# Performance work log

Measured on AMD Instinct MI355X. Metric: run time of the kernel, lower is better.

The kernel has to match this reference:

```python
import jax, jax.numpy as jnp
from jax import lax
import numpy as np

N_FEATURE = 128
EDGE = 12          # int(sqrt(128) + 1)
BATCH = 131072


def maxpool2(x):
    # 2x2 max pool, stride 2, NCHW
    return lax.reduce_window(x, -jnp.inf, lax.max,
                             (1, 1, 2, 2), (1, 1, 2, 2), 'VALID')


def conv3x3(x, w, b):
    # 3x3 conv, padding=1, NCHW / OIHW
    y = lax.conv_general_dilated(x, w, window_strides=(1, 1),
                                 padding=((1, 1), (1, 1)),
                                 dimension_numbers=('NCHW', 'OIHW', 'NCHW'))
    return y + b[None, :, None, None]


def setup_inputs() -> dict:
    key = jax.random.key(0)
    ks = jax.random.split(key, 9)
    x = jax.random.normal(ks[0], (BATCH, N_FEATURE), dtype=jnp.float32)
    conv1_w = jax.random.normal(ks[1], (3, 1, 3, 3), dtype=jnp.float32) * 0.1
    conv1_b = jnp.zeros((3,), dtype=jnp.float32)
    conv2_w = jax.random.normal(ks[2], (6, 3, 3, 3), dtype=jnp.float32) * 0.1
    conv2_b = jnp.zeros((6,), dtype=jnp.float32)
    fc1_w = jax.random.normal(ks[3], (128, 54), dtype=jnp.float32) * 0.1
    fc1_b = jnp.zeros((128,), dtype=jnp.float32)
    out_w = jax.random.normal(ks[4], (N_FEATURE, 128), dtype=jnp.float32) * 0.1
    out_b = jnp.zeros((N_FEATURE,), dtype=jnp.float32)
    return {"x": x, "conv1_w": conv1_w, "conv1_b": conv1_b,
            "conv2_w": conv2_w, "conv2_b": conv2_b,
            "fc1_w": fc1_w, "fc1_b": fc1_b,
            "out_w": out_w, "out_b": out_b}


def reference(x, conv1_w, conv1_b, conv2_w, conv2_b, fc1_w, fc1_b, out_w, out_b):
    num = x.shape[0]
    n = x.shape[1]                       # 128
    pad = EDGE * EDGE - n                # 16 trailing zeros
    # vectorized transto3D: row-major fill of edge x edge grid, zero-padded tail
    g = jnp.pad(x, ((0, 0), (0, pad))).reshape(num, 1, EDGE, EDGE)
    h = jax.nn.relu(maxpool2(conv3x3(g, conv1_w, conv1_b)))      # [num,3,6,6]
    h = jax.nn.relu(maxpool2(conv3x3(h, conv2_w, conv2_b)))      # [num,6,3,3]
    h = h.reshape(num, 54)
    h = jax.nn.relu(h @ fc1_w.T + fc1_b)                         # [num,128]
    return h @ out_w.T + out_b                                   # [num,128]
```

## Files before the change

kernel.cpp:

```cpp
#include <hip/hip_runtime.h>

typedef unsigned int uint;
typedef unsigned short ushort;

using bf16x8 = __attribute__((ext_vector_type(8))) short;
using f32x4  = __attribute__((ext_vector_type(4))) float;

__device__ __forceinline__ float b2f(ushort u) {
  union { uint i; float f; } v; v.i = ((uint)u) << 16; return v.f;
}
__device__ __forceinline__ ushort f2b(float f) {
  union { float f; uint i; } v; v.f = f;
  uint r = (v.i + 0x7fffu + ((v.i >> 16) & 1u)) >> 16;
  return (ushort)r;
}
__device__ __forceinline__ bf16x8 ldfrag(const ushort* p) {
  union { uint4 u; bf16x8 v; } x; x.u = *(const uint4*)p; return x.v;
}

__global__ __launch_bounds__(256, 1) void conv_kernel(
    const float* __restrict__ x,
    const float* __restrict__ w1g, const float* __restrict__ b1g,
    const float* __restrict__ w2g, const float* __restrict__ b2g,
    ushort* __restrict__ h2ws) {
  const int s = blockIdx.x * 256 + threadIdx.x;
  const float* xs = x + (size_t)s * 128;

  float xv[128];
#pragma unroll
  for (int i = 0; i < 32; ++i) {
    const float4 v = ((const float4*)xs)[i];
    xv[4 * i + 0] = v.x; xv[4 * i + 1] = v.y;
    xv[4 * i + 2] = v.z; xv[4 * i + 3] = v.w;
  }

  float w1[3][9], b1[3];
#pragma unroll
  for (int c = 0; c < 3; ++c) {
    b1[c] = b1g[c];
#pragma unroll
    for (int q = 0; q < 9; ++q) w1[c][q] = w1g[c * 9 + q];
  }

  float h1[3][6][6];
#pragma unroll
  for (int pr = 0; pr < 6; ++pr)
#pragma unroll
    for (int pc = 0; pc < 6; ++pc)
#pragma unroll
      for (int ch = 0; ch < 3; ++ch) {
        float m = -3.0e38f;
#pragma unroll
        for (int dr = 0; dr < 2; ++dr)
#pragma unroll
          for (int dc = 0; dc < 2; ++dc) {
            float a = 0.f;
#pragma unroll
            for (int ky = 0; ky < 3; ++ky)
#pragma unroll
              for (int kx = 0; kx < 3; ++kx) {
                const int r = 2 * pr + dr + ky - 1;
                const int c = 2 * pc + dc + kx - 1;
                if (r >= 0 && r < 12 && c >= 0 && c < 12 && (12 * r + c) < 128)
                  a = fmaf(w1[ch][ky * 3 + kx], xv[12 * r + c], a);
              }
            m = fmaxf(m, a);
          }
        h1[ch][pr][pc] = fmaxf(m + b1[ch], 0.f);
      }

  float h2[54];
#pragma unroll
  for (int o = 0; o < 6; ++o) {
    float w2[27];
#pragma unroll
    for (int q = 0; q < 27; ++q) w2[q] = w2g[o * 27 + q];
    const float bo = b2g[o];
#pragma unroll
    for (int qr = 0; qr < 3; ++qr)
#pragma unroll
      for (int qc = 0; qc < 3; ++qc) {
        float m = -3.0e38f;
#pragma unroll
        for (int dr = 0; dr < 2; ++dr)
#pragma unroll
          for (int dc = 0; dc < 2; ++dc) {
            float a = 0.f;
#pragma unroll
            for (int i = 0; i < 3; ++i)
#pragma unroll
              for (int ky = 0; ky < 3; ++ky)
#pragma unroll
                for (int kx = 0; kx < 3; ++kx) {
                  const int yy = 2 * qr + dr + ky - 1;
                  const int xx = 2 * qc + dc + kx - 1;
                  if (yy >= 0 && yy < 6 && xx >= 0 && xx < 6)
                    a = fmaf(w2[i * 9 + ky * 3 + kx], h1[i][yy][xx], a);
                }
            m = fmaxf(m, a);
          }
        h2[o * 9 + qr * 3 + qc] = fmaxf(m + bo, 0.f);
      }
  }

  uint pk[32];
#pragma unroll
  for (int q = 0; q < 27; ++q)
    pk[q] = (uint)f2b(h2[2 * q]) | ((uint)f2b(h2[2 * q + 1]) << 16);
#pragma unroll
  for (int q = 27; q < 32; ++q) pk[q] = 0u;
  uint4* dst = (uint4*)(h2ws + (size_t)s * 64);
#pragma unroll
  for (int i = 0; i < 8; ++i) {
    uint4 v; v.x = pk[4 * i]; v.y = pk[4 * i + 1];
    v.z = pk[4 * i + 2]; v.w = pk[4 * i + 3];
    dst[i] = v;
  }
}

__global__ __launch_bounds__(256, 2) void fc_kernel(
    const ushort* __restrict__ h2ws,
    const float* __restrict__ fc1w, const float* __restrict__ fc1b,
    const float* __restrict__ outw, const float* __restrict__ outb,
    float* __restrict__ out) {
  __shared__ __align__(16) union {
    struct { ushort h2s[128][72]; ushort w1s[128][72]; } p1;
    struct { ushort tA[128][136]; ushort owB[128][136]; } p2;
  } U;
  __shared__ float fb1[128], ob[128];

  const int t = threadIdx.x;
  const int s0 = blockIdx.x * 128;
  const int lane = t & 63, wv = t >> 6;
  const int quad = lane >> 4, lm = lane & 15;

  if (t < 128) { fb1[t] = fc1b[t]; ob[t] = outb[t]; }

#pragma unroll
  for (int i = 0; i < 4; ++i) {
    const int f = t + 256 * i;
    const int si = f >> 3, kb = f & 7;
    *(uint4*)&U.p1.h2s[si][kb * 8] =
        *(const uint4*)(h2ws + (size_t)(s0 + si) * 64 + kb * 8);
  }
#pragma unroll
  for (int i = 0; i < 27; ++i) {
    const int f = t + 256 * i;
    const int n = f / 54, k = f - 54 * n;
    U.p1.w1s[n][k] = f2b(fc1w[f]);
  }
  if (t < 128) {
    uint* p = (uint*)&U.p1.w1s[t][54];
#pragma unroll
    for (int q = 0; q < 5; ++q) p[q] = 0u;
  }
  __syncthreads();

  f32x4 acc[2][8];
#pragma unroll
  for (int mt = 0; mt < 2; ++mt)
#pragma unroll
    for (int nt = 0; nt < 8; ++nt) acc[mt][nt] = (f32x4){0.f, 0.f, 0.f, 0.f};

#pragma unroll
  for (int kk = 0; kk < 2; ++kk) {
    const int ko = kk * 32 + quad * 8;
    bf16x8 a[2], b[8];
#pragma unroll
    for (int mt = 0; mt < 2; ++mt)
      a[mt] = ldfrag(&U.p1.h2s[32 * wv + 16 * mt + lm][ko]);
#pragma unroll
    for (int nt = 0; nt < 8; ++nt)
      b[nt] = ldfrag(&U.p1.w1s[16 * nt + lm][ko]);
#pragma unroll
    for (int mt = 0; mt < 2; ++mt)
#pragma unroll
      for (int nt = 0; nt < 8; ++nt)
        acc[mt][nt] = __builtin_amdgcn_mfma_f32_16x16x32_bf16(
            a[mt], b[nt], acc[mt][nt], 0, 0, 0);
  }
  __syncthreads();

#pragma unroll
  for (int mt = 0; mt < 2; ++mt)
#pragma unroll
    for (int nt = 0; nt < 8; ++nt) {
      const int col = 16 * nt + lm;
      const float bj = fb1[col];
#pragma unroll
      for (int r = 0; r < 4; ++r) {
        const int row = 32 * wv + 16 * mt + quad * 4 + r;
        U.p2.tA[row][col] = f2b(fmaxf(acc[mt][nt][r] + bj, 0.f));
      }
    }
#pragma unroll
  for (int i = 0; i < 16; ++i) {
    const int f = t + 256 * i;
    const int o = f >> 5, j4 = (f & 31) * 4;
    const float4 v = *(const float4*)(outw + o * 128 + j4);
    uint2 pv;
    pv.x = (uint)f2b(v.x) | ((uint)f2b(v.y) << 16);
    pv.y = (uint)f2b(v.z) | ((uint)f2b(v.w) << 16);
    *(uint2*)&U.p2.owB[o][j4] = pv;
  }
  __syncthreads();

  f32x4 acc2[2][8];
#pragma unroll
  for (int mt = 0; mt < 2; ++mt)
#pragma unroll
    for (int nt = 0; nt < 8; ++nt) acc2[mt][nt] = (f32x4){0.f, 0.f, 0.f, 0.f};

#pragma unroll
  for (int kk = 0; kk < 4; ++kk) {
    const int ko = kk * 32 + quad * 8;
    bf16x8 a[2], b[8];
#pragma unroll
    for (int mt = 0; mt < 2; ++mt)
      a[mt] = ldfrag(&U.p2.tA[32 * wv + 16 * mt + lm][ko]);
#pragma unroll
    for (int nt = 0; nt < 8; ++nt)
      b[nt] = ldfrag(&U.p2.owB[16 * nt + lm][ko]);
#pragma unroll
    for (int mt = 0; mt < 2; ++mt)
#pragma unroll
      for (int nt = 0; nt < 8; ++nt)
        acc2[mt][nt] = __builtin_amdgcn_mfma_f32_16x16x32_bf16(
            a[mt], b[nt], acc2[mt][nt], 0, 0, 0);
  }

#pragma unroll
  for (int mt = 0; mt < 2; ++mt)
#pragma unroll
    for (int nt = 0; nt < 8; ++nt) {
      const int col = 16 * nt + lm;
      const float bo = ob[col];
#pragma unroll
      for (int r = 0; r < 4; ++r) {
        const int srow = s0 + 32 * wv + 16 * mt + quad * 4 + r;
        out[(size_t)srow * 128 + col] = acc2[mt][nt][r] + bo;
      }
    }
}

extern "C" void kernel_launch(void* const* d_in, const int* in_sizes, int n_in,
                              void* d_out, int out_size, void* d_ws, size_t ws_size,
                              hipStream_t stream) {
  const float* x    = (const float*)d_in[0];
  const float* w1   = (const float*)d_in[1];
  const float* b1   = (const float*)d_in[2];
  const float* w2   = (const float*)d_in[3];
  const float* b2   = (const float*)d_in[4];
  const float* fc1w = (const float*)d_in[5];
  const float* fc1b = (const float*)d_in[6];
  const float* outw = (const float*)d_in[7];
  const float* outb = (const float*)d_in[8];
  float* outp = (float*)d_out;
  ushort* ws  = (ushort*)d_ws;

  const int N = in_sizes[0] / 128;

  conv_kernel<<<N / 256, 256, 0, stream>>>(x, w1, b1, w2, b2, ws);
  fc_kernel<<<N / 128, 256, 0, stream>>>(ws, fc1w, fc1b, outw, outb, outp);
}
```

Baseline: 169.0 us.

## Fuse conv and FC stages into one kernel with pre-converted bf16 weights

Merges the conv kernel and the FC kernel into a single kernel that stages the pooled conv features in shared memory instead of a global workspace, then runs both MFMA GEMMs over two 128-row halves. A one-block prep kernel converts the fc1 and out weights to bf16 once per call, and the GEMM B fragments are read straight from global/L2 rather than staged in LDS. This removes the h2 global round trip and the per-block weight conversion. In exchange, the fused kernel needs more registers and LDS, which may lower occupancy, and the B-fragment loads now hit global memory.

After: 171.4 us. No clear change (+1.4%).

```diff
diff --git a/kernel.cpp b/kernel.cpp
--- a/kernel.cpp
+++ b/kernel.cpp
@@ -6,9 +6,6 @@
 using bf16x8 = __attribute__((ext_vector_type(8))) short;
 using f32x4  = __attribute__((ext_vector_type(4))) float;
 
-__device__ __forceinline__ float b2f(ushort u) {
-  union { uint i; float f; } v; v.i = ((uint)u) << 16; return v.f;
-}
 __device__ __forceinline__ ushort f2b(float f) {
   union { float f; uint i; } v; v.f = f;
   uint r = (v.i + 0x7fffu + ((v.i >> 16) & 1u)) >> 16;
@@ -18,229 +15,215 @@
   union { uint4 u; bf16x8 v; } x; x.u = *(const uint4*)p; return x.v;
 }
 
-__global__ __launch_bounds__(256, 1) void conv_kernel(
+__global__ __launch_bounds__(256) void prep_kernel(
+    const float* __restrict__ fc1w, const float* __restrict__ outw,
+    ushort* __restrict__ ws) {
+  const int t = threadIdx.x;
+#pragma unroll
+  for (int i = 0; i < 32; ++i) {
+    const int idx = t * 32 + i;
+    const int row = idx >> 6, k = idx & 63;
+    ws[idx] = (k < 54) ? f2b(fc1w[row * 54 + k]) : (ushort)0;
+  }
+#pragma unroll
+  for (int i = 0; i < 64; ++i) {
+    const int idx = t * 64 + i;
+    ws[8192 + idx] = f2b(outw[idx]);
+  }
+}
+
+__global__ __launch_bounds__(256, 2) void fused_kernel(
     const float* __restrict__ x,
     const float* __restrict__ w1g, const float* __restrict__ b1g,
     const float* __restrict__ w2g, const float* __restrict__ b2g,
-    ushort* __restrict__ h2ws) {
-  const int s = blockIdx.x * 256 + threadIdx.x;
-  const float* xs = x + (size_t)s * 128;
-
-  float xv[128];
-#pragma unroll
-  for (int i = 0; i < 32; ++i) {
-    const float4 v = ((const float4*)xs)[i];
-    xv[4 * i + 0] = v.x; xv[4 * i + 1] = v.y;
-    xv[4 * i + 2] = v.z; xv[4 * i + 3] = v.w;
-  }
-
-  float w1[3][9], b1[3];
-#pragma unroll
-  for (int c = 0; c < 3; ++c) {
-    b1[c] = b1g[c];
-#pragma unroll
-    for (int q = 0; q < 9; ++q) w1[c][q] = w1g[c * 9 + q];
-  }
-
-  float h1[3][6][6];
-#pragma unroll
-  for (int pr = 0; pr < 6; ++pr)
-#pragma unroll
-    for (int pc = 0; pc < 6; ++pc)
-#pragma unroll
-      for (int ch = 0; ch < 3; ++ch) {
-        float m = -3.0e38f;
-#pragma unroll
-        for (int dr = 0; dr < 2; ++dr)
-#pragma unroll
-          for (int dc = 0; dc < 2; ++dc) {
-            float a = 0.f;
-#pragma unroll
-            for (int ky = 0; ky < 3; ++ky)
-#pragma unroll
-              for (int kx = 0; kx < 3; ++kx) {
-                const int r = 2 * pr + dr + ky - 1;
-                const int c = 2 * pc + dc + kx - 1;
-                if (r >= 0 && r < 12 && c >= 0 && c < 12 && (12 * r + c) < 128)
-                  a = fmaf(w1[ch][ky * 3 + kx], xv[12 * r + c], a);
-              }
-            m = fmaxf(m, a);
-          }
-        h1[ch][pr][pc] = fmaxf(m + b1[ch], 0.f);
-      }
-
-  float h2[54];
-#pragma unroll
-  for (int o = 0; o < 6; ++o) {
-    float w2[27];
-#pragma unroll
-    for (int q = 0; q < 27; ++q) w2[q] = w2g[o * 27 + q];
-    const float bo = b2g[o];
-#pragma unroll
-    for (int qr = 0; qr < 3; ++qr)
-#pragma unroll
-      for (int qc = 0; qc < 3; ++qc) {
-        float m = -3.0e38f;
-#pragma unroll
-        for (int dr = 0; dr < 2; ++dr)
-#pragma unroll
-          for (int dc = 0; dc < 2; ++dc) {
-            float a = 0.f;
-#pragma unroll
-            for (int i = 0; i < 3; ++i)
+    const ushort* __restrict__ wsw,
+    const float* __restrict__ fc1b, const float* __restrict__ outb,
+    float* __restrict__ out) {
+  __shared__ __align__(16) ushort h2A[256][72];
+  __shared__ __align__(16) ushort tA[128][136];
+  __shared__ float fb1[128], ob[128];
+
+  const int t = threadIdx.x;
+  const int s0 = blockIdx.x * 256;
+
+  if (t < 128) { fb1[t] = fc1b[t]; ob[t] = outb[t]; }
+
+  {
+    const float* xs = x + (size_t)(s0 + t) * 128;
+    float xv[128];
+#pragma unroll
+    for (int i = 0; i < 32; ++i) {
+      const float4 v = ((const float4*)xs)[i];
+      xv[4 * i + 0] = v.x; xv[4 * i + 1] = v.y;
+      xv[4 * i + 2] = v.z; xv[4 * i + 3] = v.w;
+    }
+
+    float w1[3][9], b1[3];
+#pragma unroll
+    for (int c = 0; c < 3; ++c) {
+      b1[c] = b1g[c];
+#pragma unroll
+      for (int q = 0; q < 9; ++q) w1[c][q] = w1g[c * 9 + q];
+    }
+
+    float h1[3][6][6];
+#pragma unroll
+    for (int pr = 0; pr < 6; ++pr)
+#pragma unroll
+      for (int pc = 0; pc < 6; ++pc)
+#pragma unroll
+        for (int ch = 0; ch < 3; ++ch) {
+          float m = -3.0e38f;
+#pragma unroll
+          for (int dr = 0; dr < 2; ++dr)
+#pragma unroll
+            for (int dc = 0; dc < 2; ++dc) {
+              float a = 0.f;
 #pragma unroll
               for (int ky = 0; ky < 3; ++ky)
 #pragma unroll
                 for (int kx = 0; kx < 3; ++kx) {
-                  const int yy = 2 * qr + dr + ky - 1;
-                  const int xx = 2 * qc + dc + kx - 1;
-                  if (yy >= 0 && yy < 6 && xx >= 0 && xx < 6)
-                    a = fmaf(w2[i * 9 + ky * 3 + kx], h1[i][yy][xx], a);
+                  const int r = 2 * pr + dr + ky - 1;
+                  const int c = 2 * pc + dc + kx - 1;
+                  if (r >= 0 && r < 12 && c >= 0 && c < 12 && (12 * r + c) < 128)
+                    a = fmaf(w1[ch][ky * 3 + kx], xv[12 * r + c], a);
                 }
-            m = fmaxf(m, a);
-          }
-        h2[o * 9 + qr * 3 + qc] = fmaxf(m + bo, 0.f);
-      }
-  }
-
-  uint pk[32];
-#pragma unroll
-  for (int q = 0; q < 27; ++q)
-    pk[q] = (uint)f2b(h2[2 * q]) | ((uint)f2b(h2[2 * q + 1]) << 16);
-#pragma unroll
-  for (int q = 27; q < 32; ++q) pk[q] = 0u;
-  uint4* dst = (uint4*)(h2ws + (size_t)s * 64);
-#pragma unroll
-  for (int i = 0; i < 8; ++i) {
-    uint4 v; v.x = pk[4 * i]; v.y = pk[4 * i + 1];
-    v.z = pk[4 * i + 2]; v.w = pk[4 * i + 3];
-    dst[i] = v;
-  }
-}
-
-__global__ __launch_bounds__(256, 2) void fc_kernel(
-    const ushort* __restrict__ h2ws,
-    const float* __restrict__ fc1w, const float* __restrict__ fc1b,
-    const float* __restrict__ outw, const float* __restrict__ outb,
-    float* __restrict__ out) {
-  __shared__ __align__(16) union {
-    struct { ushort h2s[128][72]; ushort w1s[128][72]; } p1;
-    struct { ushort tA[128][136]; ushort owB[128][136]; } p2;
-  } U;
-  __shared__ float fb1[128], ob[128];
-
-  const int t = threadIdx.x;
-  const int s0 = blockIdx.x * 128;
+              m = fmaxf(m, a);
+            }
+          h1[ch][pr][pc] = fmaxf(m + b1[ch], 0.f);
+        }
+
+    float h2[54];
+#pragma unroll
+    for (int o = 0; o < 6; ++o) {
+      float w2[27];
+#pragma unroll
+      for (int q = 0; q < 27; ++q) w2[q] = w2g[o * 27 + q];
+      const float bo = b2g[o];
+#pragma unroll
+      for (int qr = 0; qr < 3; ++qr)
+#pragma unroll
+        for (int qc = 0; qc < 3; ++qc) {
+          float m = -3.0e38f;
+#pragma unroll
+          for (int dr = 0; dr < 2; ++dr)
+#pragma unroll
+            for (int dc = 0; dc < 2; ++dc) {
+              float a = 0.f;
+#pragma unroll
+              for (int i = 0; i < 3; ++i)
+#pragma unroll
+                for (int ky = 0; ky < 3; ++ky)
+#pragma unroll
+                  for (int kx = 0; kx < 3; ++kx) {
+                    const int yy = 2 * qr + dr + ky - 1;
+                    const int xx = 2 * qc + dc + kx - 1;
+                    if (yy >= 0 && yy < 6 && xx >= 0 && xx < 6)
+                      a = fmaf(w2[i * 9 + ky * 3 + kx], h1[i][yy][xx], a);
+                  }
+              m = fmaxf(m, a);
+            }
+          h2[o * 9 + qr * 3 + qc] = fmaxf(m + bo, 0.f);
+        }
+    }
+
+    uint pk[32];
+#pragma unroll
+    for (int q = 0; q < 27; ++q)
+      pk[q] = (uint)f2b(h2[2 * q]) | ((uint)f2b(h2[2 * q + 1]) << 16);
+#pragma unroll
+    for (int q = 27; q < 32; ++q) pk[q] = 0u;
+#pragma unroll
+    for (int i = 0; i < 8; ++i) {
+      uint4 v; v.x = pk[4 * i]; v.y = pk[4 * i + 1];
+      v.z = pk[4 * i + 2]; v.w = pk[4 * i + 3];
+      *(uint4*)&h2A[t][8 * i] = v;
+    }
+  }
+  __syncthreads();
+
   const int lane = t & 63, wv = t >> 6;
   const int quad = lane >> 4, lm = lane & 15;
-
-  if (t < 128) { fb1[t] = fc1b[t]; ob[t] = outb[t]; }
-
-#pragma unroll
-  for (int i = 0; i < 4; ++i) {
-    const int f = t + 256 * i;
-    const int si = f >> 3, kb = f & 7;
-    *(uint4*)&U.p1.h2s[si][kb * 8] =
-        *(const uint4*)(h2ws + (size_t)(s0 + si) * 64 + kb * 8);
-  }
-#pragma unroll
-  for (int i = 0; i < 27; ++i) {
-    const int f = t + 256 * i;
-    const int n = f / 54, k = f - 54 * n;
-    U.p1.w1s[n][k] = f2b(fc1w[f]);
-  }
-  if (t < 128) {
-    uint* p = (uint*)&U.p1.w1s[t][54];
-#pragma unroll
-    for (int q = 0; q < 5; ++q) p[q] = 0u;
-  }
-  __syncthreads();
-
-  f32x4 acc[2][8];
-#pragma unroll
-  for (int mt = 0; mt < 2; ++mt)
-#pragma unroll
-    for (int nt = 0; nt < 8; ++nt) acc[mt][nt] = (f32x4){0.f, 0.f, 0.f, 0.f};
-
-#pragma unroll
-  for (int kk = 0; kk < 2; ++kk) {
-    const int ko = kk * 32 + quad * 8;
-    bf16x8 a[2], b[8];
-#pragma unroll
-    for (int mt = 0; mt < 2; ++mt)
-      a[mt] = ldfrag(&U.p1.h2s[32 * wv + 16 * mt + lm][ko]);
-#pragma unroll
-    for (int nt = 0; nt < 8; ++nt)
-      b[nt] = ldfrag(&U.p1.w1s[16 * nt + lm][ko]);
-#pragma unroll
-    for (int mt = 0; mt < 2; ++mt)
+  const ushort* wsA = wsw;
+  const ushort* wsB = wsw + 8192;
+
+  for (int h = 0; h < 2; ++h) {
+    f32x4 acc[2][8];
+#pragma unroll
+    for (int mt = 0; mt < 2; ++mt)
+#pragma unroll
+      for (int nt = 0; nt < 8; ++nt) acc[mt][nt] = (f32x4){0.f, 0.f, 0.f, 0.f};
+
+#pragma unroll
+    for (int kk = 0; kk < 2; ++kk) {
+      const int ko = kk * 32 + quad * 8;
+      bf16x8 a[2], b[8];
+#pragma unroll
+      for (int mt = 0; mt < 2; ++mt)
+        a[mt] = ldfrag(&h2A[128 * h + 32 * wv + 16 * mt + lm][ko]);
 #pragma unroll
       for (int nt = 0; nt < 8; ++nt)
-        acc[mt][nt] = __builtin_amdgcn_mfma_f32_16x16x32_bf16(
-            a[mt], b[nt], acc[mt][nt], 0, 0, 0);
-  }
-  __syncthreads();
-
-#pragma unroll
-  for (int mt = 0; mt < 2; ++mt)
-#pragma unroll
-    for (int nt = 0; nt < 8; ++nt) {
-      const int col = 16 * nt + lm;
-      const float bj = fb1[col];
-#pragma unroll
-      for (int r = 0; r < 4; ++r) {
-        const int row = 32 * wv + 16 * mt + quad * 4 + r;
-        U.p2.tA[row][col] = f2b(fmaxf(acc[mt][nt][r] + bj, 0.f));
+        b[nt] = ldfrag(wsA + (16 * nt + lm) * 64 + ko);
+#pragma unroll
+      for (int mt = 0; mt < 2; ++mt)
+#pragma unroll
+        for (int nt = 0; nt < 8; ++nt)
+          acc[mt][nt] = __builtin_amdgcn_mfma_f32_16x16x32_bf16(
+              a[mt], b[nt], acc[mt][nt], 0, 0, 0);
+    }
+
+#pragma unroll
+    for (int mt = 0; mt < 2; ++mt)
+#pragma unroll
+      for (int nt = 0; nt < 8; ++nt) {
+        const int col = 16 * nt + lm;
+        const float bj = fb1[col];
+#pragma unroll
+        for (int r = 0; r < 4; ++r) {
+          const int row = 32 * wv + 16 * mt + quad * 4 + r;
+          tA[row][col] = f2b(fmaxf(acc[mt][nt][r] + bj, 0.f));
+        }
       }
-    }
-#pragma unroll
-  for (int i = 0; i < 16; ++i) {
-    const int f = t + 256 * i;
-    const int o = f >> 5, j4 = (f & 31) * 4;
-    const float4 v = *(const float4*)(outw + o * 128 + j4);
-    uint2 pv;
-    pv.x = (uint)f2b(v.x) | ((uint)f2b(v.y) << 16);
-    pv.y = (uint)f2b(v.z) | ((uint)f2b(v.w) << 16);
-    *(uint2*)&U.p2.owB[o][j4] = pv;
-  }
-  __syncthreads();
-
-  f32x4 acc2[2][8];
-#pragma unroll
-  for (int mt = 0; mt < 2; ++mt)
-#pragma unroll
-    for (int nt = 0; nt < 8; ++nt) acc2[mt][nt] = (f32x4){0.f, 0.f, 0.f, 0.f};
-
-#pragma unroll
-  for (int kk = 0; kk < 4; ++kk) {
-    const int ko = kk * 32 + quad * 8;
-    bf16x8 a[2], b[8];
-#pragma unroll
-    for (int mt = 0; mt < 2; ++mt)
-      a[mt] = ldfrag(&U.p2.tA[32 * wv + 16 * mt + lm][ko]);
-#pragma unroll
-    for (int nt = 0; nt < 8; ++nt)
-      b[nt] = ldfrag(&U.p2.owB[16 * nt + lm][ko]);
-#pragma unroll
-    for (int mt = 0; mt < 2; ++mt)
+    __syncthreads();
+
+    f32x4 acc2[2][8];
+#pragma unroll
+    for (int mt = 0; mt < 2; ++mt)
+#pragma unroll
+      for (int nt = 0; nt < 8; ++nt) acc2[mt][nt] = (f32x4){0.f, 0.f, 0.f, 0.f};
+
+#pragma unroll
+    for (int kk = 0; kk < 4; ++kk) {
+      const int ko = kk * 32 + quad * 8;
+      bf16x8 a[2], b[8];
+#pragma unroll
+      for (int mt = 0; mt < 2; ++mt)
+        a[mt] = ldfrag(&tA[32 * wv + 16 * mt + lm][ko]);
 #pragma unroll
       for (int nt = 0; nt < 8; ++nt)
-        acc2[mt][nt] = __builtin_amdgcn_mfma_f32_16x16x32_bf16(
-            a[mt], b[nt], acc2[mt][nt], 0, 0, 0);
-  }
-
-#pragma unroll
-  for (int mt = 0; mt < 2; ++mt)
-#pragma unroll
-    for (int nt = 0; nt < 8; ++nt) {
-      const int col = 16 * nt + lm;
-      const float bo = ob[col];
-#pragma unroll
-      for (int r = 0; r < 4; ++r) {
-        const int srow = s0 + 32 * wv + 16 * mt + quad * 4 + r;
-        out[(size_t)srow * 128 + col] = acc2[mt][nt][r] + bo;
+        b[nt] = ldfrag(wsB + (16 * nt + lm) * 128 + ko);
+#pragma unroll
+      for (int mt = 0; mt < 2; ++mt)
+#pragma unroll
+        for (int nt = 0; nt < 8; ++nt)
+          acc2[mt][nt] = __builtin_amdgcn_mfma_f32_16x16x32_bf16(
+              a[mt], b[nt], acc2[mt][nt], 0, 0, 0);
+    }
+
+#pragma unroll
+    for (int mt = 0; mt < 2; ++mt)
+#pragma unroll
+      for (int nt = 0; nt < 8; ++nt) {
+        const int col = 16 * nt + lm;
+        const float bo = ob[col];
+#pragma unroll
+        for (int r = 0; r < 4; ++r) {
+          const int srow = s0 + 128 * h + 32 * wv + 16 * mt + quad * 4 + r;
+          out[(size_t)srow * 128 + col] = acc2[mt][nt][r] + bo;
+        }
       }
-    }
+    __syncthreads();
+  }
 }
 
 extern "C" void kernel_launch(void* const* d_in, const int* in_sizes, int n_in,
@@ -260,6 +243,7 @@
 
   const int N = in_sizes[0] / 128;
 
-  conv_kernel<<<N / 256, 256, 0, stream>>>(x, w1, b1, w2, b2, ws);
-  fc_kernel<<<N / 128, 256, 0, stream>>>(ws, fc1w, fc1b, outw, outb, outp);
-}
+  prep_kernel<<<1, 256, 0, stream>>>(fc1w, outw, ws);
+  fused_kernel<<<N / 256, 256, 0, stream>>>(x, w1, b1, w2, b2, ws,
+                                            fc1b, outb, outp);
+}
```
